# Kernel optimization log

Hardware: AMD Instinct MI355X
Metric: run time of the kernel (lower is better)

## Reference

```python
import jax, jax.numpy as jnp
import numpy as np

D = 1024   # hidden_dim
F = 4096   # ffn_dim
E = 8      # expert_num
K = 2      # top_k
B, S = 2, 2048

def setup_inputs() -> dict:
    key = jax.random.key(0)
    ks = jax.random.split(key, 5)
    scale = 0.02
    x = jax.random.normal(ks[0], (B, S, D), dtype=jnp.float32)
    gate_w = jax.random.normal(ks[1], (D, E), dtype=jnp.float32) * scale
    w1 = jax.random.normal(ks[2], (E, D, F), dtype=jnp.float32) * scale
    w3 = jax.random.normal(ks[3], (E, D, F), dtype=jnp.float32) * scale
    w2 = jax.random.normal(ks[4], (E, F, D), dtype=jnp.float32) * scale
    return {"x": x, "gate_w": gate_w, "w1": w1, "w3": w3, "w2": w2}

def reference(x, gate_w, w1, w3, w2):
    # x: [B, S, D] -> tokens [T, D]
    Bb, Ss, Dd = x.shape
    xt = x.reshape(-1, Dd)                                  # [T, D]
    T = xt.shape[0]
    # Router: softmax over experts in float32 (matches torch dtype=torch.float)
    router_probs = jax.nn.softmax((xt @ gate_w).astype(jnp.float32), axis=-1)  # [T, E]
    topk_w, topk_idx = jax.lax.top_k(router_probs, K)        # [T, K]
    topk_w = topk_w / topk_w.sum(axis=-1, keepdims=True)
    topk_w = topk_w.astype(x.dtype)
    # Combine weights scattered to dense [T, E] (equivalent to per-expert gather/scatter loop)
    combine = jnp.zeros((T, E), dtype=x.dtype).at[jnp.arange(T)[:, None], topk_idx].add(topk_w)
    # SwishFFN per expert: w2(silu(x w1) * (x w3)), no bias
    h = jax.nn.silu(jnp.einsum('td,edf->etf', xt, w1)) * jnp.einsum('td,edf->etf', xt, w3)  # [E, T, F]
    out_e = jnp.einsum('etf,efd->etd', h, w2)                # [E, T, D]
    out = jnp.einsum('etd,te->td', out_e, combine)           # [T, D]
    return out.reshape(Bb, Ss, Dd), router_probs
```

## Files before the change

### kernel.cpp

```cpp
#include <hip/hip_runtime.h>

typedef unsigned short u16;
typedef unsigned int u32;
typedef __attribute__((ext_vector_type(8))) short bf16x8;
typedef __attribute__((ext_vector_type(4))) float f32x4;
typedef __attribute__((ext_vector_type(4))) int i32x4;
typedef __attribute__((ext_vector_type(2))) unsigned int u32x2;


__device__ __forceinline__ u16 f2bf(float f) {
  u32 u = __builtin_bit_cast(u32, f);
  u += 0x7fffu + ((u >> 16) & 1u);
  return (u16)(u >> 16);
}
__device__ __forceinline__ u32 pack2(u16 a, u16 b) { return (u32)a | ((u32)b << 16); }

__device__ __forceinline__ char* lds_swz(void* base, int row, int byteInRow) {
  return (char*)base + (((row << 7) + byteInRow) ^ ((row & 7) << 4));
}

#define GLL16(g, l) __builtin_amdgcn_global_load_lds( \
    (const __attribute__((address_space(1))) void*)(g), \
    (__attribute__((address_space(3))) void*)(l), 16, 0, 0)

__device__ __forceinline__ void trans_tiles(
    const float* __restrict__ src, u16* __restrict__ dst,
    int Cs, int Rs, int c0, int r0base, int NT, float* lds )
{
  const int tid = threadIdx.x;
  const int w = tid >> 6, l = tid & 63;
  const float* sbase = src + (size_t)(r0base + w * 16 + (l >> 4)) * Cs + c0 + (l & 15) * 4;
  const int c = tid & 63, rseg = tid >> 6;

#pragma unroll
  for (int q = 0; q < 4; ++q)
    GLL16(sbase + (size_t)(q * 4) * Cs, lds + (w * 16 + q * 4) * 64);

  for (int t = 0; t < NT; ++t) {
    if (t + 1 < NT) {
      const float* sb2 = sbase + (size_t)((t + 1) * 64) * Cs;
      float* lb2 = lds + ((t + 1) & 1) * 4096;
#pragma unroll
      for (int q = 0; q < 4; ++q)
        GLL16(sb2 + (size_t)(q * 4) * Cs, lb2 + (w * 16 + q * 4) * 64);
      asm volatile("s_waitcnt vmcnt(4)" ::: "memory");
    } else {
      asm volatile("s_waitcnt vmcnt(0)" ::: "memory");
    }
    __builtin_amdgcn_s_barrier();
    const float* tb = lds + (t & 1) * 4096;
    u32 p[8];
#pragma unroll
    for (int i = 0; i < 8; ++i) {
      float a  = tb[(rseg * 16 + 2 * i) * 64 + c];
      float bv = tb[(rseg * 16 + 2 * i + 1) * 64 + c];
      p[i] = pack2(f2bf(a), f2bf(bv));
    }
    u16* dp = dst + (size_t)(c0 + c) * Rs + r0base + t * 64 + rseg * 16;
    *(i32x4*)dp = *(i32x4*)&p[0];
    *(i32x4*)(dp + 8) = *(i32x4*)&p[4];
    asm volatile("s_waitcnt lgkmcnt(0)" ::: "memory");
    __builtin_amdgcn_s_barrier();
  }
}

__global__ __launch_bounds__(256) void prep_k(
    const float* __restrict__ w1, const float* __restrict__ w3,
    u16* __restrict__ w1t, u16* __restrict__ w3t,
    const float* __restrict__ x, const float* __restrict__ gw,
    float* __restrict__ probs, u16* __restrict__ xb,
    float* __restrict__ wa, int* __restrict__ alist, int* __restrict__ cnt)
{
  __shared__ __align__(16) float smem[2][4096];
  const int bid = blockIdx.x;
  if (bid >= 4096) {
    const int t0 = bid - 4096;
    const int sel = t0 >> 10;
    const int rem = t0 & 1023;
    const int e = rem >> 7;
    const int rem2 = rem & 127;
    const int ct = rem2 >> 1;
    const int rh = rem2 & 1;
    const float* src = (sel ? w3 : w1) + (size_t)e * 4194304;
    u16* dst = (sel ? w3t : w1t) + (size_t)e * 4194304;
    trans_tiles(src, dst, 4096, 1024, ct * 64, rh * 512, 8, &smem[0][0]);
    return;
  }
  const int t = bid;
  const int tid = threadIdx.x;
  f32x4 xv = ((const f32x4*)(x + (size_t)t * 1024))[tid];
  u32x2 hb;
  hb[0] = pack2(f2bf(xv[0]), f2bf(xv[1]));
  hb[1] = pack2(f2bf(xv[2]), f2bf(xv[3]));
  *(u32x2*)(xb + (size_t)t * 1024 + tid * 4) = hb;

  float acc[8];
#pragma unroll
  for (int e = 0; e < 8; ++e) acc[e] = 0.f;
  const float* g = gw + tid * 32;
#pragma unroll
  for (int j = 0; j < 4; ++j)
#pragma unroll
    for (int e = 0; e < 8; ++e) acc[e] = fmaf(xv[j], g[j * 8 + e], acc[e]);

#pragma unroll
  for (int e = 0; e < 8; ++e)
    for (int off = 32; off > 0; off >>= 1) acc[e] += __shfl_down(acc[e], off);

  float* red = &smem[0][0];
  const int lane = tid & 63, wid = tid >> 6;
  if (lane == 0) {
#pragma unroll
    for (int e = 0; e < 8; ++e) red[wid * 8 + e] = acc[e];
  }
  __syncthreads();
  if (tid == 0) {
    float p[8]; float mx = -1e30f;
#pragma unroll
    for (int e = 0; e < 8; ++e) { p[e] = red[e] + red[8 + e] + red[16 + e] + red[24 + e]; mx = fmaxf(mx, p[e]); }
    float s = 0.f;
#pragma unroll
    for (int e = 0; e < 8; ++e) { p[e] = __expf(p[e] - mx); s += p[e]; }
    float inv = 1.f / s;
#pragma unroll
    for (int e = 0; e < 8; ++e) { p[e] *= inv; probs[(size_t)t * 8 + e] = p[e]; }
    int i0 = 0;
#pragma unroll
    for (int e = 1; e < 8; ++e) if (p[e] > p[i0]) i0 = e;
    int i1 = (i0 == 0) ? 1 : 0;
#pragma unroll
    for (int e = 0; e < 8; ++e) if (e != i0 && p[e] > p[i1]) i1 = e;
    float s2 = p[i0] + p[i1];
    int pos0 = atomicAdd(&cnt[i0], 1); alist[i0 * 4096 + pos0] = t * 2;
    int pos1 = atomicAdd(&cnt[i1], 1); alist[i1 * 4096 + pos1] = t * 2 + 1;
    wa[t * 2]     = p[i0] / s2;
    wa[t * 2 + 1] = p[i1] / s2;
  }
}

__global__ __launch_bounds__(256, 2) void gemm1w2_k(
    const u16* __restrict__ xb, const u16* __restrict__ w1t, const u16* __restrict__ w3t,
    const int* __restrict__ alist, const int* __restrict__ cnt, u16* __restrict__ H,
    const float* __restrict__ w2, u16* __restrict__ w2t)
{
  __shared__ __align__(16) char smem[33280];
  const int e = blockIdx.z;
  const int bx = blockIdx.x;

  if (bx >= 64) {
    const int slot = (bx - 64) * 256 + blockIdx.y * 8 + e;
    const int e2 = slot >> 8;
    const int idx = slot & 255;
    const float* src = w2 + (size_t)e2 * 4194304;
    u16* dst = w2t + (size_t)e2 * 4194304;
    trans_tiles(src, dst, 1024, 4096, (idx >> 4) * 64, (idx & 15) * 256, 4, (float*)smem);
    return;
  }

  u16* As = (u16*)smem;
  u16* Bs = (u16*)(smem + 16384);
  int* rowid = (int*)(smem + 32768);

  const int mc = cnt[e];
  const int m0 = blockIdx.y * 128;
  if (m0 >= mc) return;
  const int n0 = bx * 64;
  const int tid = threadIdx.x;

  if (tid < 128) rowid[tid] = (m0 + tid < mc) ? alist[e * 4096 + m0 + tid] : -1;
  __syncthreads();

  const int l = tid & 63, w = tid >> 6;
  const u16* wt = (w >> 1) ? w3t : w1t;
  u16* bbase = Bs + (w >> 1) * 4096;

  const u16* aps[4]; const u16* bps[4];
  u16* ald[4]; u16* bld[4];
#pragma unroll
  for (int q = 0; q < 4; ++q) {
    int ra = 32 * w + 8 * q + (l >> 3);
    int id = rowid[ra];
    aps[q] = xb + (size_t)(id < 0 ? 0 : (id >> 1)) * 1024 + ((l & 7) ^ (ra & 7)) * 8;
    ald[q] = As + (32 * w + 8 * q) * 64;
    int rb = 32 * (w & 1) + 8 * q + (l >> 3);
    bps[q] = wt + (size_t)e * 4194304 + (size_t)(n0 + rb) * 1024 + ((l & 7) ^ (rb & 7)) * 8;
    bld[q] = bbase + (32 * (w & 1) + 8 * q) * 64;
  }

  const int wm = (w >> 1) * 64, wn = (w & 1) * 32;
  const int l15 = l & 15, lg = l >> 4;

  f32x4 acc1[4][2], acc3[4][2];
  const f32x4 zf = {0.f, 0.f, 0.f, 0.f};
#pragma unroll
  for (int mi = 0; mi < 4; ++mi) { acc1[mi][0] = zf; acc1[mi][1] = zf; acc3[mi][0] = zf; acc3[mi][1] = zf; }

  for (int kt = 0; kt < 16; ++kt) {
    const int ko = kt * 64;
#pragma unroll
    for (int q = 0; q < 4; ++q) GLL16(aps[q] + ko, ald[q]);
#pragma unroll
    for (int q = 0; q < 4; ++q) GLL16(bps[q] + ko, bld[q]);
    __syncthreads();
#pragma unroll
    for (int ks = 0; ks < 2; ++ks) {
      const int kb = ks * 64 + lg * 16;
      bf16x8 af[4];
#pragma unroll
      for (int mi = 0; mi < 4; ++mi)
        af[mi] = *(const bf16x8*)lds_swz(As, wm + mi * 16 + l15, kb);
#pragma unroll
      for (int ni = 0; ni < 2; ++ni) {
        bf16x8 b1 = *(const bf16x8*)lds_swz(Bs, wn + ni * 16 + l15, kb);
        bf16x8 b3 = *(const bf16x8*)lds_swz(Bs + 4096, wn + ni * 16 + l15, kb);
#pragma unroll
        for (int mi = 0; mi < 4; ++mi) {
          acc1[mi][ni] = __builtin_amdgcn_mfma_f32_16x16x32_bf16(af[mi], b1, acc1[mi][ni], 0, 0, 0);
          acc3[mi][ni] = __builtin_amdgcn_mfma_f32_16x16x32_bf16(af[mi], b3, acc3[mi][ni], 0, 0, 0);
        }
      }
    }
    __syncthreads();
  }

#pragma unroll
  for (int mi = 0; mi < 4; ++mi) {
    const int rb = wm + mi * 16 + lg * 4;
#pragma unroll
    for (int ni = 0; ni < 2; ++ni) {
      const int col = n0 + wn + ni * 16 + l15;
      f32x4 c1 = acc1[mi][ni], c3 = acc3[mi][ni];
#pragma unroll
      for (int j = 0; j < 4; ++j) {
        int id = rowid[rb + j];
        if (id >= 0) {
          float a = c1[j];
          float h = (a / (1.f + __expf(-a))) * c3[j];
          H[(size_t)id * 4096 + col] = f2bf(h);
        }
      }
    }
  }
}

__global__ __launch_bounds__(256, 2) void gemm2_k(
    const u16* __restrict__ H, const u16* __restrict__ w2t,
    const int* __restrict__ alist, const int* __restrict__ cnt,
    const float* __restrict__ wa, float* __restrict__ out)
{
  const int e = blockIdx.z;
  const int mc = cnt[e];
  const int yy = blockIdx.y;
  const int kh = yy & 1;
  const int m0 = (yy >> 1) * 128;
  if (m0 >= mc) return;
  const int n0 = blockIdx.x * 128;
  const int tid = threadIdx.x;

  __shared__ u16 As[128 * 64];
  __shared__ u16 Bs[128 * 64];
  __shared__ int rowid[128];
  __shared__ float rw[128];

  if (tid < 128) {
    int id = (m0 + tid < mc) ? alist[e * 4096 + m0 + tid] : -1;
    rowid[tid] = id;
    rw[tid] = (id >= 0) ? wa[id] : 0.f;
  }
  __syncthreads();

  const int l = tid & 63, w = tid >> 6;
  const size_t kbase = (size_t)kh * 2048;
  const u16* aps[4]; const u16* bps[4];
  u16* ald[4]; u16* bld[4];
#pragma unroll
  for (int q = 0; q < 4; ++q) {
    int ra = 32 * w + 8 * q + (l >> 3);
    int id = rowid[ra];
    aps[q] = H + (size_t)(id < 0 ? 0 : id) * 4096 + kbase + ((l & 7) ^ (ra & 7)) * 8;
    ald[q] = As + (32 * w + 8 * q) * 64;
    int rb = 32 * w + 8 * q + (l >> 3);
    bps[q] = w2t + (size_t)e * 4194304 + (size_t)(n0 + rb) * 4096 + kbase + ((l & 7) ^ (rb & 7)) * 8;
    bld[q] = Bs + (32 * w + 8 * q) * 64;
  }

  const int wm = (w >> 1) * 64, wn = (w & 1) * 64;
  const int l15 = l & 15, lg = l >> 4;

  f32x4 acc[4][4];
  const f32x4 zf = {0.f, 0.f, 0.f, 0.f};
#pragma unroll
  for (int mi = 0; mi < 4; ++mi)
#pragma unroll
    for (int ni = 0; ni < 4; ++ni) acc[mi][ni] = zf;

  for (int kt = 0; kt < 32; ++kt) {
    const int ko = kt * 64;
#pragma unroll
    for (int q = 0; q < 4; ++q) GLL16(aps[q] + ko, ald[q]);
#pragma unroll
    for (int q = 0; q < 4; ++q) GLL16(bps[q] + ko, bld[q]);
    __syncthreads();
#pragma unroll
    for (int ks = 0; ks < 2; ++ks) {
      const int kb = ks * 64 + lg * 16;
      bf16x8 af[4];
#pragma unroll
      for (int mi = 0; mi < 4; ++mi)
        af[mi] = *(const bf16x8*)lds_swz(As, wm + mi * 16 + l15, kb);
#pragma unroll
      for (int ni = 0; ni < 4; ++ni) {
        bf16x8 bfb = *(const bf16x8*)lds_swz(Bs, wn + ni * 16 + l15, kb);
#pragma unroll
        for (int mi = 0; mi < 4; ++mi)
          acc[mi][ni] = __builtin_amdgcn_mfma_f32_16x16x32_bf16(af[mi], bfb, acc[mi][ni], 0, 0, 0);
      }
    }
    __syncthreads();
  }

#pragma unroll
  for (int mi = 0; mi < 4; ++mi) {
    const int rb = wm + mi * 16 + lg * 4;
#pragma unroll
    for (int ni = 0; ni < 4; ++ni) {
      const int col = n0 + wn + ni * 16 + l15;
      f32x4 c = acc[mi][ni];
#pragma unroll
      for (int j = 0; j < 4; ++j) {
        int rr = rb + j;
        int id = rowid[rr];
        if (id >= 0)
          unsafeAtomicAdd(&out[(size_t)(id >> 1) * 1024 + col], c[j] * rw[rr]);
      }
    }
  }
}

extern "C" void kernel_launch(void* const* d_in, const int* in_sizes, int n_in,
                              void* d_out, int out_size, void* d_ws, size_t ws_size,
                              hipStream_t stream)
{
  (void)in_sizes; (void)n_in; (void)out_size; (void)ws_size;
  const float* x  = (const float*)d_in[0];
  const float* gw = (const float*)d_in[1];
  const float* w1 = (const float*)d_in[2];
  const float* w3 = (const float*)d_in[3];
  const float* w2 = (const float*)d_in[4];
  float* out   = (float*)d_out;
  float* probs = out + (size_t)4096 * 1024;

  const size_t MB = (size_t)1 << 20;
  char* ws = (char*)d_ws;
  u16*   xb    = (u16*)(ws);
  u16*   H     = (u16*)(ws + 8 * MB);
  u16*   w1t   = (u16*)(ws + 72 * MB);
  u16*   w3t   = (u16*)(ws + 136 * MB);
  u16*   w2t   = (u16*)(ws + 200 * MB);
  float* wa    = (float*)(ws + 264 * MB);
  int*   alist = (int*)(ws + 264 * MB + 32768);
  int*   cnt   = (int*)(ws + 264 * MB + 32768 + 131072);

  hipMemsetAsync(cnt, 0, 8 * sizeof(int), stream);
  hipMemsetAsync(out, 0, (size_t)4096 * 1024 * sizeof(float), stream);
  prep_k<<<6144, 256, 0, stream>>>(w1, w3, w1t, w3t, x, gw, probs, xb, wa, alist, cnt);
  gemm1w2_k<<<dim3(72, 32, 8), 256, 0, stream>>>(xb, w1t, w3t, alist, cnt, H, w2, w2t);
  gemm2_k<<<dim3(8, 64, 8), 256, 0, stream>>>(H, w2t, alist, cnt, wa, out);
}
```

Baseline: 510.5 us.

## Split weight transposition across stages to overlap with first GEMM

Instead of transposing all of w1/w3 in the prep kernel, only the first 16 column tiles (1024 of 4096 ffn columns) are transposed there. The first GEMM then runs on that slice while extra blocks transpose the rest, and a third launch finishes GEMM1 for the remaining columns alongside the w2 transpose. The goal is to hide the fp32-to-bf16 weight conversion behind useful GEMM work rather than running it serially. In exchange there is one more kernel launch and each stage carries a mixed workload that can be unevenly balanced.

```diff
diff --git a/kernel.cpp b/kernel.cpp
--- a/kernel.cpp
+++ b/kernel.cpp
@@ -64,99 +64,11 @@
   }
 }
 
-__global__ __launch_bounds__(256) void prep_k(
-    const float* __restrict__ w1, const float* __restrict__ w3,
-    u16* __restrict__ w1t, u16* __restrict__ w3t,
-    const float* __restrict__ x, const float* __restrict__ gw,
-    float* __restrict__ probs, u16* __restrict__ xb,
-    float* __restrict__ wa, int* __restrict__ alist, int* __restrict__ cnt)
-{
-  __shared__ __align__(16) float smem[2][4096];
-  const int bid = blockIdx.x;
-  if (bid >= 4096) {
-    const int t0 = bid - 4096;
-    const int sel = t0 >> 10;
-    const int rem = t0 & 1023;
-    const int e = rem >> 7;
-    const int rem2 = rem & 127;
-    const int ct = rem2 >> 1;
-    const int rh = rem2 & 1;
-    const float* src = (sel ? w3 : w1) + (size_t)e * 4194304;
-    u16* dst = (sel ? w3t : w1t) + (size_t)e * 4194304;
-    trans_tiles(src, dst, 4096, 1024, ct * 64, rh * 512, 8, &smem[0][0]);
-    return;
-  }
-  const int t = bid;
-  const int tid = threadIdx.x;
-  f32x4 xv = ((const f32x4*)(x + (size_t)t * 1024))[tid];
-  u32x2 hb;
-  hb[0] = pack2(f2bf(xv[0]), f2bf(xv[1]));
-  hb[1] = pack2(f2bf(xv[2]), f2bf(xv[3]));
-  *(u32x2*)(xb + (size_t)t * 1024 + tid * 4) = hb;
-
-  float acc[8];
-#pragma unroll
-  for (int e = 0; e < 8; ++e) acc[e] = 0.f;
-  const float* g = gw + tid * 32;
-#pragma unroll
-  for (int j = 0; j < 4; ++j)
-#pragma unroll
-    for (int e = 0; e < 8; ++e) acc[e] = fmaf(xv[j], g[j * 8 + e], acc[e]);
-
-#pragma unroll
-  for (int e = 0; e < 8; ++e)
-    for (int off = 32; off > 0; off >>= 1) acc[e] += __shfl_down(acc[e], off);
-
-  float* red = &smem[0][0];
-  const int lane = tid & 63, wid = tid >> 6;
-  if (lane == 0) {
-#pragma unroll
-    for (int e = 0; e < 8; ++e) red[wid * 8 + e] = acc[e];
-  }
-  __syncthreads();
-  if (tid == 0) {
-    float p[8]; float mx = -1e30f;
-#pragma unroll
-    for (int e = 0; e < 8; ++e) { p[e] = red[e] + red[8 + e] + red[16 + e] + red[24 + e]; mx = fmaxf(mx, p[e]); }
-    float s = 0.f;
-#pragma unroll
-    for (int e = 0; e < 8; ++e) { p[e] = __expf(p[e] - mx); s += p[e]; }
-    float inv = 1.f / s;
-#pragma unroll
-    for (int e = 0; e < 8; ++e) { p[e] *= inv; probs[(size_t)t * 8 + e] = p[e]; }
-    int i0 = 0;
-#pragma unroll
-    for (int e = 1; e < 8; ++e) if (p[e] > p[i0]) i0 = e;
-    int i1 = (i0 == 0) ? 1 : 0;
-#pragma unroll
-    for (int e = 0; e < 8; ++e) if (e != i0 && p[e] > p[i1]) i1 = e;
-    float s2 = p[i0] + p[i1];
-    int pos0 = atomicAdd(&cnt[i0], 1); alist[i0 * 4096 + pos0] = t * 2;
-    int pos1 = atomicAdd(&cnt[i1], 1); alist[i1 * 4096 + pos1] = t * 2 + 1;
-    wa[t * 2]     = p[i0] / s2;
-    wa[t * 2 + 1] = p[i1] / s2;
-  }
-}
-
-__global__ __launch_bounds__(256, 2) void gemm1w2_k(
-    const u16* __restrict__ xb, const u16* __restrict__ w1t, const u16* __restrict__ w3t,
+__device__ __forceinline__ void gemm1_body(
+    char* smem, const u16* __restrict__ xb, const u16* __restrict__ w1t, const u16* __restrict__ w3t,
     const int* __restrict__ alist, const int* __restrict__ cnt, u16* __restrict__ H,
-    const float* __restrict__ w2, u16* __restrict__ w2t)
-{
-  __shared__ __align__(16) char smem[33280];
-  const int e = blockIdx.z;
-  const int bx = blockIdx.x;
-
-  if (bx >= 64) {
-    const int slot = (bx - 64) * 256 + blockIdx.y * 8 + e;
-    const int e2 = slot >> 8;
-    const int idx = slot & 255;
-    const float* src = w2 + (size_t)e2 * 4194304;
-    u16* dst = w2t + (size_t)e2 * 4194304;
-    trans_tiles(src, dst, 1024, 4096, (idx >> 4) * 64, (idx & 15) * 256, 4, (float*)smem);
-    return;
-  }
-
+    int e, int nbase)
+{
   u16* As = (u16*)smem;
   u16* Bs = (u16*)(smem + 16384);
   int* rowid = (int*)(smem + 32768);
@@ -164,7 +76,7 @@
   const int mc = cnt[e];
   const int m0 = blockIdx.y * 128;
   if (m0 >= mc) return;
-  const int n0 = bx * 64;
+  const int n0 = (nbase + blockIdx.x) * 64;
   const int tid = threadIdx.x;
 
   if (tid < 128) rowid[tid] = (m0 + tid < mc) ? alist[e * 4096 + m0 + tid] : -1;
@@ -241,6 +153,123 @@
       }
     }
   }
+}
+
+__global__ __launch_bounds__(256) void l1_k(
+    const float* __restrict__ w1, const float* __restrict__ w3,
+    u16* __restrict__ w1t, u16* __restrict__ w3t,
+    const float* __restrict__ x, const float* __restrict__ gw,
+    float* __restrict__ probs, u16* __restrict__ xb,
+    float* __restrict__ wa, int* __restrict__ alist, int* __restrict__ cnt)
+{
+  __shared__ __align__(16) float smem[2][4096];
+  const int bid = blockIdx.x;
+  if (bid >= 4096) {
+    const int t0 = bid - 4096;
+    const int sel = t0 >> 8;
+    const int rem = t0 & 255;
+    const int e = rem >> 5;
+    const int rem2 = rem & 31;
+    const int ct = rem2 >> 1;
+    const int rh = rem2 & 1;
+    const float* src = (sel ? w3 : w1) + (size_t)e * 4194304;
+    u16* dst = (sel ? w3t : w1t) + (size_t)e * 4194304;
+    trans_tiles(src, dst, 4096, 1024, ct * 64, rh * 512, 8, &smem[0][0]);
+    return;
+  }
+  const int t = bid;
+  const int tid = threadIdx.x;
+  f32x4 xv = ((const f32x4*)(x + (size_t)t * 1024))[tid];
+  u32x2 hb;
+  hb[0] = pack2(f2bf(xv[0]), f2bf(xv[1]));
+  hb[1] = pack2(f2bf(xv[2]), f2bf(xv[3]));
+  *(u32x2*)(xb + (size_t)t * 1024 + tid * 4) = hb;
+
+  float acc[8];
+#pragma unroll
+  for (int e = 0; e < 8; ++e) acc[e] = 0.f;
+  const float* g = gw + tid * 32;
+#pragma unroll
+  for (int j = 0; j < 4; ++j)
+#pragma unroll
+    for (int e = 0; e < 8; ++e) acc[e] = fmaf(xv[j], g[j * 8 + e], acc[e]);
+
+#pragma unroll
+  for (int e = 0; e < 8; ++e)
+    for (int off = 32; off > 0; off >>= 1) acc[e] += __shfl_down(acc[e], off);
+
+  float* red = &smem[0][0];
+  const int lane = tid & 63, wid = tid >> 6;
+  if (lane == 0) {
+#pragma unroll
+    for (int e = 0; e < 8; ++e) red[wid * 8 + e] = acc[e];
+  }
+  __syncthreads();
+  if (tid == 0) {
+    float p[8]; float mx = -1e30f;
+#pragma unroll
+    for (int e = 0; e < 8; ++e) { p[e] = red[e] + red[8 + e] + red[16 + e] + red[24 + e]; mx = fmaxf(mx, p[e]); }
+    float s = 0.f;
+#pragma unroll
+    for (int e = 0; e < 8; ++e) { p[e] = __expf(p[e] - mx); s += p[e]; }
+    float inv = 1.f / s;
+#pragma unroll
+    for (int e = 0; e < 8; ++e) { p[e] *= inv; probs[(size_t)t * 8 + e] = p[e]; }
+    int i0 = 0;
+#pragma unroll
+    for (int e = 1; e < 8; ++e) if (p[e] > p[i0]) i0 = e;
+    int i1 = (i0 == 0) ? 1 : 0;
+#pragma unroll
+    for (int e = 0; e < 8; ++e) if (e != i0 && p[e] > p[i1]) i1 = e;
+    float s2 = p[i0] + p[i1];
+    int pos0 = atomicAdd(&cnt[i0], 1); alist[i0 * 4096 + pos0] = t * 2;
+    int pos1 = atomicAdd(&cnt[i1], 1); alist[i1 * 4096 + pos1] = t * 2 + 1;
+    wa[t * 2]     = p[i0] / s2;
+    wa[t * 2 + 1] = p[i1] / s2;
+  }
+}
+
+__global__ __launch_bounds__(256, 2) void l2_k(
+    const u16* __restrict__ xb, const u16* __restrict__ w1t, const u16* __restrict__ w3t,
+    const int* __restrict__ alist, const int* __restrict__ cnt, u16* __restrict__ H,
+    const float* __restrict__ w1, const float* __restrict__ w3,
+    u16* __restrict__ w1to, u16* __restrict__ w3to)
+{
+  __shared__ __align__(16) char smem[33280];
+  const int bx = blockIdx.x;
+  if (bx >= 16) {
+    const int slot = (bx - 16) * 256 + blockIdx.y * 8 + blockIdx.z;
+    const int sel = slot >= 768;
+    const int r = sel ? (slot - 768) : slot;
+    const int e = r / 96;
+    const int r2 = r - e * 96;
+    const int ct = 16 + (r2 >> 1);
+    const int rh = r2 & 1;
+    const float* src = (sel ? w3 : w1) + (size_t)e * 4194304;
+    u16* dst = (sel ? w3to : w1to) + (size_t)e * 4194304;
+    trans_tiles(src, dst, 4096, 1024, ct * 64, rh * 512, 8, (float*)smem);
+    return;
+  }
+  gemm1_body(smem, xb, w1t, w3t, alist, cnt, H, blockIdx.z, 0);
+}
+
+__global__ __launch_bounds__(256, 2) void l3_k(
+    const u16* __restrict__ xb, const u16* __restrict__ w1t, const u16* __restrict__ w3t,
+    const int* __restrict__ alist, const int* __restrict__ cnt, u16* __restrict__ H,
+    const float* __restrict__ w2, u16* __restrict__ w2t)
+{
+  __shared__ __align__(16) char smem[33280];
+  const int bx = blockIdx.x;
+  if (bx >= 48) {
+    const int slot = (bx - 48) * 256 + blockIdx.y * 8 + blockIdx.z;
+    const int e2 = slot >> 8;
+    const int idx = slot & 255;
+    const float* src = w2 + (size_t)e2 * 4194304;
+    u16* dst = w2t + (size_t)e2 * 4194304;
+    trans_tiles(src, dst, 1024, 4096, (idx >> 4) * 64, (idx & 15) * 256, 4, (float*)smem);
+    return;
+  }
+  gemm1_body(smem, xb, w1t, w3t, alist, cnt, H, blockIdx.z, 16);
 }
 
 __global__ __launch_bounds__(256, 2) void gemm2_k(
@@ -363,7 +392,8 @@
 
   hipMemsetAsync(cnt, 0, 8 * sizeof(int), stream);
   hipMemsetAsync(out, 0, (size_t)4096 * 1024 * sizeof(float), stream);
-  prep_k<<<6144, 256, 0, stream>>>(w1, w3, w1t, w3t, x, gw, probs, xb, wa, alist, cnt);
-  gemm1w2_k<<<dim3(72, 32, 8), 256, 0, stream>>>(xb, w1t, w3t, alist, cnt, H, w2, w2t);
+  l1_k<<<4608, 256, 0, stream>>>(w1, w3, w1t, w3t, x, gw, probs, xb, wa, alist, cnt);
+  l2_k<<<dim3(22, 32, 8), 256, 0, stream>>>(xb, w1t, w3t, alist, cnt, H, w1, w3, w1t, w3t);
+  l3_k<<<dim3(56, 32, 8), 256, 0, stream>>>(xb, w1t, w3t, alist, cnt, H, w2, w2t);
   gemm2_k<<<dim3(8, 64, 8), 256, 0, stream>>>(H, w2t, alist, cnt, wa, out);
 }
```

Measured after the change: 544.2 us. +6.6%, slower.
